# Optimization experiments

Hardware: AMD Instinct MI355X
Metric: run time of the kernel (lower is better)

The kernel has to match this reference:

```python
import jax, jax.numpy as jnp
import numpy as np

# Static config matching init_kwargs
SPATIAL_SCALE = 0.25
SAMPLING_RATIO = 2
PH, PW = 7, 7
ALIGNED = True
CLOCKWISE = False


def setup_inputs() -> dict:
    key = jax.random.key(0)
    k_feat, k_b, k_c, k_wh, k_a = jax.random.split(key, 5)
    N, C, H, W = 2, 256, 256, 256
    n_rois = 1024
    feat = jax.random.normal(k_feat, (N, C, H, W), dtype=jnp.float32)
    # rois: (batch_idx, cx, cy, w, h, angle) in IMAGE coordinates (stride-4 map)
    b = jax.random.randint(k_b, (n_rois,), 0, N).astype(jnp.float32)
    ctr = jax.random.uniform(k_c, (n_rois, 2), minval=0.0, maxval=1024.0)
    wh = jax.random.uniform(k_wh, (n_rois, 2), minval=32.0, maxval=320.0)
    ang = jax.random.uniform(k_a, (n_rois,), minval=-np.pi, maxval=np.pi)
    rois = jnp.concatenate([b[:, None], ctr, wh, ang[:, None]], axis=1).astype(jnp.float32)
    return {"input": feat, "rois": rois}


def _roi_align_rotated(feat, rois):
    N, C, H, W = feat.shape
    b = rois[:, 0].astype(jnp.int32)
    off = 0.5 if ALIGNED else 0.0
    cx = rois[:, 1] * SPATIAL_SCALE - off
    cy = rois[:, 2] * SPATIAL_SCALE - off
    rw = rois[:, 3] * SPATIAL_SCALE
    rh = rois[:, 4] * SPATIAL_SCALE
    th = -rois[:, 5] if CLOCKWISE else rois[:, 5]
    if not ALIGNED:
        rw = jnp.maximum(rw, 1.0)
        rh = jnp.maximum(rh, 1.0)
    bin_h = rh / PH  # [n]
    bin_w = rw / PW
    gh = gw = SAMPLING_RATIO  # sampling_ratio > 0 -> static grid

    py = jnp.arange(PH, dtype=feat.dtype)
    px = jnp.arange(PW, dtype=feat.dtype)
    sy = (jnp.arange(gh, dtype=feat.dtype) + 0.5) / gh
    sx = (jnp.arange(gw, dtype=feat.dtype) + 0.5) / gw
    # roi-local sample coords: yy [n,PH,gh], xx [n,PW,gw]
    yy = (-rh / 2)[:, None, None] + (py[None, :, None] + sy[None, None, :]) * bin_h[:, None, None]
    xx = (-rw / 2)[:, None, None] + (px[None, :, None] + sx[None, None, :]) * bin_w[:, None, None]
    # broadcast to [n,PH,PW,gh,gw]
    yy5 = yy[:, :, None, :, None]
    xx5 = xx[:, None, :, None, :]
    cos = jnp.cos(th)[:, None, None, None, None]
    sin = jnp.sin(th)[:, None, None, None, None]
    cyb = cy[:, None, None, None, None]
    cxb = cx[:, None, None, None, None]
    # mmcv convention: y = yy*cos - xx*sin + cy ; x = yy*sin + xx*cos + cx
    y = yy5 * cos - xx5 * sin + cyb
    x = yy5 * sin + xx5 * cos + cxb

    valid = (y > -1.0) & (y < H) & (x > -1.0) & (x < W)
    y = jnp.maximum(y, 0.0)
    x = jnp.maximum(x, 0.0)
    yl = y.astype(jnp.int32)
    xl = x.astype(jnp.int32)
    condy = yl >= H - 1
    condx = xl >= W - 1
    yl = jnp.where(condy, H - 1, yl)
    xl = jnp.where(condx, W - 1, xl)
    yh = jnp.minimum(yl + 1, H - 1)
    xh = jnp.minimum(xl + 1, W - 1)
    y = jnp.where(condy, yl.astype(y.dtype), y)
    x = jnp.where(condx, xl.astype(x.dtype), x)
    ly = y - yl
    lx = x - xl
    hy = 1.0 - ly
    hx = 1.0 - lx

    b5 = b[:, None, None, None, None]

    def gather(yi, xi):
        # -> [n,PH,PW,gh,gw,C]
        return feat[b5, :, yi, xi]

    v = ((hy * hx)[..., None] * gather(yl, xl)
         + (hy * lx)[..., None] * gather(yl, xh)
         + (ly * hx)[..., None] * gather(yh, xl)
         + (ly * lx)[..., None] * gather(yh, xh))
    v = jnp.where(valid[..., None], v, 0.0)
    out = v.mean(axis=(3, 4))  # average over the gh*gw samples -> [n,PH,PW,C]
    return jnp.transpose(out, (0, 3, 1, 2))  # [n,C,PH,PW]


def reference(input, rois):
    return _roi_align_rotated(input, rois)
```

## Files before the change

kernel.cpp:

```cpp
#include <hip/hip_runtime.h>

#define SPATIAL_SCALE 0.25f
#define PH_ 7
#define PW_ 7
#define NBINS 49
#define NSAMP 196
#define C_ 256
#define H_ 256
#define W_ 256
#define HW_ (H_ * W_)
#define RES_STRIDE 257

__global__ __launch_bounds__(256) void transpose_nchw_nhwc(
    const float* __restrict__ in, float* __restrict__ out) {
  __shared__ float tile[32][33];
  const int b  = blockIdx.z;
  const int c0 = blockIdx.y * 32;
  const int p0 = blockIdx.x * 32;
  const float* src = in  + (size_t)b * C_ * HW_;
  float*       dst = out + (size_t)b * HW_ * C_;
  const int tx = threadIdx.x;
  const int ty = threadIdx.y;
#pragma unroll
  for (int i = 0; i < 32; i += 8)
    tile[ty + i][tx] = src[(size_t)(c0 + ty + i) * HW_ + p0 + tx];
  __syncthreads();
#pragma unroll
  for (int i = 0; i < 32; i += 8)
    dst[(size_t)(p0 + ty + i) * C_ + c0 + tx] = tile[tx][ty + i];
}

template <bool NHWC>
__global__ __launch_bounds__(256) void roi_align_rotated_kernel(
    const float* __restrict__ feat, const float* __restrict__ rois,
    float* __restrict__ out) {
  __shared__ int4   d_off[NSAMP];
  __shared__ float4 d_w[NSAMP];
  __shared__ float  res[NBINS * RES_STRIDE];

  const int r = blockIdx.x;
  const int t = threadIdx.x;

  if (t < NSAMP) {
    const float* rp = rois + r * 6;
    const int   b  = (int)rp[0];
    const float cx = rp[1] * SPATIAL_SCALE - 0.5f;
    const float cy = rp[2] * SPATIAL_SCALE - 0.5f;
    const float rw = rp[3] * SPATIAL_SCALE;
    const float rh = rp[4] * SPATIAL_SCALE;
    const float th = rp[5];
    float sn, cs;
    sincosf(th, &sn, &cs);
    const float bin_h = rh / (float)PH_;
    const float bin_w = rw / (float)PW_;

    const int s   = t;
    const int bin = s >> 2;
    const int sub = s & 3;
    const int ph  = bin / 7;
    const int pw  = bin - ph * 7;
    const int iy  = sub >> 1;
    const int ix  = sub & 1;

    const float yy = -0.5f * rh + ((float)ph + ((float)iy + 0.5f) * 0.5f) * bin_h;
    const float xx = -0.5f * rw + ((float)pw + ((float)ix + 0.5f) * 0.5f) * bin_w;
    float y = yy * cs - xx * sn + cy;
    float x = yy * sn + xx * cs + cx;

    const bool valid = (y > -1.0f) && (y < (float)H_) &&
                       (x > -1.0f) && (x < (float)W_);
    y = fminf(fmaxf(y, 0.0f), (float)(H_ - 1));
    x = fminf(fmaxf(x, 0.0f), (float)(W_ - 1));
    const int yl = (int)y;
    const int xl = (int)x;
    const int yh = min(yl + 1, H_ - 1);
    const int xh = min(xl + 1, W_ - 1);
    const float ly = y - (float)yl, lx = x - (float)xl;
    const float hy = 1.0f - ly, hx = 1.0f - lx;
    float w11 = hy * hx, w12 = hy * lx, w21 = ly * hx, w22 = ly * lx;
    if (!valid) { w11 = w12 = w21 = w22 = 0.0f; }

    int4 off;
    if (NHWC) {
      off.x = ((b * H_ + yl) * W_ + xl) * C_;
      off.y = ((b * H_ + yl) * W_ + xh) * C_;
      off.z = ((b * H_ + yh) * W_ + xl) * C_;
      off.w = ((b * H_ + yh) * W_ + xh) * C_;
    } else {
      const int base = b * C_ * HW_;
      off.x = base + yl * W_ + xl;
      off.y = base + yl * W_ + xh;
      off.z = base + yh * W_ + xl;
      off.w = base + yh * W_ + xh;
    }
    d_off[s] = off;
    d_w[s]   = make_float4(w11, w12, w21, w22);
  }
  __syncthreads();

  const int c    = t;
  const int coff = NHWC ? c : c * HW_;
  for (int bin = 0; bin < NBINS; ++bin) {
    float acc = 0.0f;
#pragma unroll
    for (int sub = 0; sub < 4; ++sub) {
      const int4   o = d_off[bin * 4 + sub];
      const float4 w = d_w[bin * 4 + sub];
      acc += w.x * feat[o.x + coff];
      acc += w.y * feat[o.y + coff];
      acc += w.z * feat[o.z + coff];
      acc += w.w * feat[o.w + coff];
    }
    res[bin * RES_STRIDE + c] = acc * 0.25f;
  }
  __syncthreads();

  float* outr = out + (size_t)r * (C_ * NBINS);
#pragma unroll 1
  for (int i = t; i < C_ * NBINS; i += 256) {
    const int cc = i / NBINS;
    const int bb = i - cc * NBINS;
    outr[i] = res[bb * RES_STRIDE + cc];
  }
}

extern "C" void kernel_launch(void* const* d_in, const int* in_sizes, int n_in,
                              void* d_out, int out_size, void* d_ws, size_t ws_size,
                              hipStream_t stream) {
  const float* feat = (const float*)d_in[0];
  const float* rois = (const float*)d_in[1];
  float* out = (float*)d_out;
  const int n_rois  = in_sizes[1] / 6;
  const int n_batch = in_sizes[0] / (C_ * HW_);

  const size_t need = (size_t)n_batch * C_ * HW_ * sizeof(float);
  if (ws_size >= need) {
    float* feat_t = (float*)d_ws;
    dim3 tb(32, 8);
    dim3 tg(HW_ / 32, C_ / 32, n_batch);
    hipLaunchKernelGGL(transpose_nchw_nhwc, tg, tb, 0, stream, feat, feat_t);
    hipLaunchKernelGGL((roi_align_rotated_kernel<true>), dim3(n_rois), dim3(256),
                       0, stream, feat_t, rois, out);
  } else {
    hipLaunchKernelGGL((roi_align_rotated_kernel<false>), dim3(n_rois), dim3(256),
                       0, stream, feat, rois, out);
  }
}
```

Before: 315.8 us.

## Vectorize NHWC transpose and ROI gather with float4, chunk bins through smaller LDS

The transpose now uses register-level 4x4 float4 transposes with no shared memory. The NHWC ROI kernel assigns each wave a bin and each lane four channels, loading float4 vectors from the gathered corners. Results are staged in a 16-bin LDS buffer and written out chunk by chunk, which cuts shared memory use to allow four blocks per CU. The aim is fewer memory instructions and higher occupancy, at the cost of more barriers and a separate tail path for the last bin.

```diff
diff --git a/kernel.cpp b/kernel.cpp
--- a/kernel.cpp
+++ b/kernel.cpp
@@ -9,38 +9,36 @@
 #define H_ 256
 #define W_ 256
 #define HW_ (H_ * W_)
-#define RES_STRIDE 257
+#define RES_STRIDE 264
+#define CHUNK 16
 
 __global__ __launch_bounds__(256) void transpose_nchw_nhwc(
     const float* __restrict__ in, float* __restrict__ out) {
-  __shared__ float tile[32][33];
-  const int b  = blockIdx.z;
-  const int c0 = blockIdx.y * 32;
-  const int p0 = blockIdx.x * 32;
+  const int b    = blockIdx.z;
+  const int p0   = blockIdx.x * 256;
+  const int c0   = blockIdx.y * 16;
+  const int lane = threadIdx.x & 63;
+  const int w    = threadIdx.x >> 6;
+  const int p    = p0 + lane * 4;
+  const int c    = c0 + w * 4;
   const float* src = in  + (size_t)b * C_ * HW_;
   float*       dst = out + (size_t)b * HW_ * C_;
-  const int tx = threadIdx.x;
-  const int ty = threadIdx.y;
-#pragma unroll
-  for (int i = 0; i < 32; i += 8)
-    tile[ty + i][tx] = src[(size_t)(c0 + ty + i) * HW_ + p0 + tx];
-  __syncthreads();
-#pragma unroll
-  for (int i = 0; i < 32; i += 8)
-    dst[(size_t)(p0 + ty + i) * C_ + c0 + tx] = tile[tx][ty + i];
+
+  const float4 r0 = *(const float4*)(src + (size_t)(c + 0) * HW_ + p);
+  const float4 r1 = *(const float4*)(src + (size_t)(c + 1) * HW_ + p);
+  const float4 r2 = *(const float4*)(src + (size_t)(c + 2) * HW_ + p);
+  const float4 r3 = *(const float4*)(src + (size_t)(c + 3) * HW_ + p);
+
+  *(float4*)(dst + (size_t)(p + 0) * C_ + c) = make_float4(r0.x, r1.x, r2.x, r3.x);
+  *(float4*)(dst + (size_t)(p + 1) * C_ + c) = make_float4(r0.y, r1.y, r2.y, r3.y);
+  *(float4*)(dst + (size_t)(p + 2) * C_ + c) = make_float4(r0.z, r1.z, r2.z, r3.z);
+  *(float4*)(dst + (size_t)(p + 3) * C_ + c) = make_float4(r0.w, r1.w, r2.w, r3.w);
 }
 
 template <bool NHWC>
-__global__ __launch_bounds__(256) void roi_align_rotated_kernel(
-    const float* __restrict__ feat, const float* __restrict__ rois,
-    float* __restrict__ out) {
-  __shared__ int4   d_off[NSAMP];
-  __shared__ float4 d_w[NSAMP];
-  __shared__ float  res[NBINS * RES_STRIDE];
-
-  const int r = blockIdx.x;
-  const int t = threadIdx.x;
-
+__device__ inline void compute_descriptors(const float* __restrict__ rois,
+                                           int r, int t,
+                                           int4* d_off, float4* d_w) {
   if (t < NSAMP) {
     const float* rp = rois + r * 6;
     const int   b  = (int)rp[0];
@@ -96,10 +94,94 @@
     d_off[s] = off;
     d_w[s]   = make_float4(w11, w12, w21, w22);
   }
+}
+
+__global__ __launch_bounds__(256, 4) void roi_align_rotated_nhwc(
+    const float* __restrict__ feat, const float* __restrict__ rois,
+    float* __restrict__ out) {
+  __shared__ int4   d_off[NSAMP];
+  __shared__ float4 d_w[NSAMP];
+  __shared__ float  res[CHUNK * RES_STRIDE];
+
+  const int r = blockIdx.x;
+  const int t = threadIdx.x;
+
+  compute_descriptors<true>(rois, r, t, d_off, d_w);
   __syncthreads();
 
+  const int w  = t >> 6;
+  const int c4 = (t & 63) * 4;
+  float* outr = out + (size_t)r * (C_ * NBINS);
+
+  for (int chunk = 0; chunk < 3; ++chunk) {
+    const int b0 = chunk * CHUNK;
+    for (int it = 0; it < CHUNK; it += 4) {
+      const int bin = b0 + it + w;
+      float4 acc = make_float4(0.f, 0.f, 0.f, 0.f);
+#pragma unroll
+      for (int sub = 0; sub < 4; ++sub) {
+        const int4   o  = d_off[bin * 4 + sub];
+        const float4 wt = d_w[bin * 4 + sub];
+        const float4 vx = *(const float4*)(feat + o.x + c4);
+        const float4 vy = *(const float4*)(feat + o.y + c4);
+        const float4 vz = *(const float4*)(feat + o.z + c4);
+        const float4 vw = *(const float4*)(feat + o.w + c4);
+        acc.x += wt.x * vx.x + wt.y * vy.x + wt.z * vz.x + wt.w * vw.x;
+        acc.y += wt.x * vx.y + wt.y * vy.y + wt.z * vz.y + wt.w * vw.y;
+        acc.z += wt.x * vx.z + wt.y * vy.z + wt.z * vz.z + wt.w * vw.z;
+        acc.w += wt.x * vx.w + wt.y * vy.w + wt.z * vz.w + wt.w * vw.w;
+      }
+      const int bl = it + w;
+      *(float4*)(&res[bl * RES_STRIDE + c4]) =
+          make_float4(acc.x * 0.25f, acc.y * 0.25f, acc.z * 0.25f, acc.w * 0.25f);
+    }
+    __syncthreads();
+#pragma unroll 1
+    for (int i = t; i < C_ * CHUNK; i += 256) {
+      const int cc = i >> 4;
+      const int bb = i & 15;
+      outr[cc * NBINS + b0 + bb] = res[bb * RES_STRIDE + cc];
+    }
+    __syncthreads();
+  }
+
+  if (w == 0) {
+    const int bin = 48;
+    float4 acc = make_float4(0.f, 0.f, 0.f, 0.f);
+#pragma unroll
+    for (int sub = 0; sub < 4; ++sub) {
+      const int4   o  = d_off[bin * 4 + sub];
+      const float4 wt = d_w[bin * 4 + sub];
+      const float4 vx = *(const float4*)(feat + o.x + c4);
+      const float4 vy = *(const float4*)(feat + o.y + c4);
+      const float4 vz = *(const float4*)(feat + o.z + c4);
+      const float4 vw = *(const float4*)(feat + o.w + c4);
+      acc.x += wt.x * vx.x + wt.y * vy.x + wt.z * vz.x + wt.w * vw.x;
+      acc.y += wt.x * vx.y + wt.y * vy.y + wt.z * vz.y + wt.w * vw.y;
+      acc.z += wt.x * vx.z + wt.y * vy.z + wt.z * vz.z + wt.w * vw.z;
+      acc.w += wt.x * vx.w + wt.y * vy.w + wt.z * vz.w + wt.w * vw.w;
+    }
+    outr[(c4 + 0) * NBINS + bin] = acc.x * 0.25f;
+    outr[(c4 + 1) * NBINS + bin] = acc.y * 0.25f;
+    outr[(c4 + 2) * NBINS + bin] = acc.z * 0.25f;
+    outr[(c4 + 3) * NBINS + bin] = acc.w * 0.25f;
+  }
+}
+
+__global__ __launch_bounds__(256) void roi_align_rotated_nchw(
+    const float* __restrict__ feat, const float* __restrict__ rois,
+    float* __restrict__ out) {
+  __shared__ int4   d_off[NSAMP];
+  __shared__ float4 d_w[NSAMP];
+  __shared__ float  res[NBINS * 257];
+
+  const int r = blockIdx.x;
+  const int t = threadIdx.x;
+  compute_descriptors<false>(rois, r, t, d_off, d_w);
+  __syncthreads();
+
   const int c    = t;
-  const int coff = NHWC ? c : c * HW_;
+  const int coff = c * HW_;
   for (int bin = 0; bin < NBINS; ++bin) {
     float acc = 0.0f;
 #pragma unroll
@@ -111,7 +193,7 @@
       acc += w.z * feat[o.z + coff];
       acc += w.w * feat[o.w + coff];
     }
-    res[bin * RES_STRIDE + c] = acc * 0.25f;
+    res[bin * 257 + c] = acc * 0.25f;
   }
   __syncthreads();
 
@@ -120,7 +202,7 @@
   for (int i = t; i < C_ * NBINS; i += 256) {
     const int cc = i / NBINS;
     const int bb = i - cc * NBINS;
-    outr[i] = res[bb * RES_STRIDE + cc];
+    outr[i] = res[bb * 257 + cc];
   }
 }
 
@@ -136,13 +218,13 @@
   const size_t need = (size_t)n_batch * C_ * HW_ * sizeof(float);
   if (ws_size >= need) {
     float* feat_t = (float*)d_ws;
-    dim3 tb(32, 8);
-    dim3 tg(HW_ / 32, C_ / 32, n_batch);
+    dim3 tb(256);
+    dim3 tg(HW_ / 256, C_ / 16, n_batch);
     hipLaunchKernelGGL(transpose_nchw_nhwc, tg, tb, 0, stream, feat, feat_t);
-    hipLaunchKernelGGL((roi_align_rotated_kernel<true>), dim3(n_rois), dim3(256),
+    hipLaunchKernelGGL(roi_align_rotated_nhwc, dim3(n_rois), dim3(256),
                        0, stream, feat_t, rois, out);
   } else {
-    hipLaunchKernelGGL((roi_align_rotated_kernel<false>), dim3(n_rois), dim3(256),
+    hipLaunchKernelGGL(roi_align_rotated_nchw, dim3(n_rois), dim3(256),
                        0, stream, feat, rois, out);
   }
 }
```

Result: slower. 367.7 us (+16.4%).
